# Optimization experiments

Measured on AMD Instinct MI355X. Metric: run time of the kernel, lower is better.

The kernel has to match this reference:

```python
import jax, jax.numpy as jnp
import numpy as np

B, L, S, H, E = 2, 2048, 2048, 16, 64


def setup_inputs() -> dict:
    key = jax.random.key(0)
    kq, kk, kv = jax.random.split(key, 3)
    queries = jax.random.normal(kq, (B, L, H, E), dtype=jnp.float32)
    keys = jax.random.normal(kk, (B, S, H, E), dtype=jnp.float32)
    values = jax.random.normal(kv, (B, S, H, E), dtype=jnp.float32)
    attn_mask = jnp.ones((B, 1, L, S), dtype=jnp.float32)  # >0.5 means attend
    return {"queries": queries, "keys": keys, "values": values, "attn_mask": attn_mask}


def reference(queries, keys, values, attn_mask):
    # queries: [B,L,H,E], keys/values: [B,S,H,E], attn_mask broadcastable to [B,H,L,S]
    E_ = queries.shape[-1]
    scale = 1.0 / np.sqrt(E_).astype(np.float32)
    scores = jnp.einsum('blhe,bshe->bhls', queries, keys)  # [B,H,L,S]
    large_negative = jnp.float32(-1e9)
    scores = scores + jnp.where(attn_mask > 0.5, jnp.float32(0.0), large_negative)
    A = jax.nn.softmax(scale * scores, axis=-1)  # dropout p=0.0 -> identity
    V = jnp.einsum('bhls,bshd->bhld', A, values)  # [B,H,L,D]
    return V
```

## Files before the change

### kernel.cpp

```cpp
#include <hip/hip_runtime.h>

typedef float    f32x4 __attribute__((ext_vector_type(4)));
typedef _Float16 f16x2 __attribute__((ext_vector_type(2)));
typedef _Float16 f16x4 __attribute__((ext_vector_type(4)));
typedef _Float16 f16x8 __attribute__((ext_vector_type(8)));
typedef int      i32x4 __attribute__((ext_vector_type(4)));

namespace {
constexpr int B_ = 2, L_ = 2048, S_ = 2048, H_ = 16, E_ = 64;
constexpr int MBLK = 128;
constexpr int NT = 64;
constexpr int NTILES = S_ / NT;

#define SCALE2f 0.1803368801111204f
#define MBIAS2f -1.8033688e8f

constexpr size_t KHOFF = (size_t)1 << 20;
constexpr size_t VHOFF = KHOFF + (size_t)B_ * H_ * S_ * E_ * 2;

__device__ __forceinline__ f16x2 cvt2(float a, float b) {
  return __builtin_bit_cast(f16x2, __builtin_amdgcn_cvt_pkrtz(a, b));
}
__device__ __forceinline__ int pkh(float a, float b) {
  return __builtin_bit_cast(int, __builtin_amdgcn_cvt_pkrtz(a, b));
}
union H8 { f16x8 v; i32x4 i; };
union H4 { f16x4 v; f16x2 h[2]; };

#define GLOAD_LDS16(g, l)                                              \
  __builtin_amdgcn_global_load_lds(                                    \
      (const __attribute__((address_space(1))) void*)(g),              \
      (__attribute__((address_space(3))) void*)(l), 16, 0, 0)
}

extern "C" __global__ __launch_bounds__(256)
void maskpack_kernel(const float* __restrict__ Mg, unsigned long long* __restrict__ Wb) {
  const int u = blockIdx.x * 256 + threadIdx.x;
  const float* src = Mg + (size_t)u * 16;
  unsigned m = 0;
#pragma unroll
  for (int i = 0; i < 4; ++i) {
    f32x4 x = *(const f32x4*)(src + i * 4);
#pragma unroll
    for (int c = 0; c < 4; ++c) m |= (x[c] > 0.5f ? 1u : 0u) << (i * 4 + c);
  }
  ((unsigned short*)Wb)[u] = (unsigned short)m;
}

extern "C" __global__ __launch_bounds__(256)
void kcvt_kernel(const float* __restrict__ Kg, _Float16* __restrict__ Kh) {
  const int idx = blockIdx.x * 256 + threadIdx.x;
  const int j = idx & 7;
  const int h = (idx >> 3) & (H_ - 1);
  const int s = (idx >> 7) & (S_ - 1);
  const int b = idx >> 18;
  const float* src = Kg + ((((size_t)b * S_ + s) * H_ + h) << 6) + j * 8;
  f32x4 x = *(const f32x4*)src, y = *(const f32x4*)(src + 4);
  i32x4 w = {pkh(x[0], x[1]), pkh(x[2], x[3]), pkh(y[0], y[1]), pkh(y[2], y[3])};
  *(i32x4*)(Kh + ((((size_t)b * H_ + h) * S_ + s) << 6) + j * 8) = w;
}

extern "C" __global__ __launch_bounds__(256)
void vcvt_kernel(const float* __restrict__ Vg, _Float16* __restrict__ Vh) {
  __shared__ _Float16 T[64][72];
  const int bid = blockIdx.x;
  const int st = bid & 31;
  const int h  = (bid >> 5) & (H_ - 1);
  const int b  = bid >> 9;
  const int t  = threadIdx.x;
  const int sl = t >> 2;
  const int e0 = (t & 3) << 4;
  const float* src = Vg + ((((size_t)b * S_ + st * 64 + sl) * H_ + h) << 6) + e0;
#pragma unroll
  for (int i = 0; i < 4; ++i) {
    f32x4 x = *(const f32x4*)(src + i * 4);
#pragma unroll
    for (int c = 0; c < 4; ++c) T[e0 + i * 4 + c][sl] = (_Float16)x[c];
  }
  __syncthreads();
  const int er = t >> 2;
  const int s0 = (t & 3) << 4;
  _Float16* dst = Vh + (((((size_t)b * H_ + h) << 6) + er) * S_) + st * 64 + s0;
  *(i32x4*)dst       = *(const i32x4*)&T[er][s0];
  *(i32x4*)(dst + 8) = *(const i32x4*)&T[er][s0 + 8];
}

extern "C" __global__ __launch_bounds__(512, 4)
void fattn_kernel(const float* __restrict__ Qg, const _Float16* __restrict__ Kh,
                  const _Float16* __restrict__ Vh, const unsigned long long* __restrict__ Wb,
                  float* __restrict__ Og) {
  __shared__ __align__(16) _Float16 Ks[2][NT][64];
  __shared__ __align__(16) _Float16 Vt[2][E_][64];

  const int tid  = threadIdx.x;
  const int wv   = tid >> 6;
  const int lane = tid & 63;
  const int qd   = lane >> 4;
  const int cl   = lane & 15;
  const int sw   = cl & 7;

  const int bid = blockIdx.x;
  const int qb  = bid >> 5;
  const int bh  = bid & 31;
  const int h   = bh & (H_ - 1);
  const int b   = bh >> 4;

  const int l0 = qb * MBLK + wv * 16;

  f16x8 qf[2];
  {
    const float* qp = Qg + ((((size_t)b * L_ + (l0 + cl)) * H_ + h) << 6);
#pragma unroll
    for (int kb = 0; kb < 2; ++kb) {
      const int e0 = qd * 8 + kb * 32;
      f32x4 x = *(const f32x4*)(qp + e0);
      f32x4 y = *(const f32x4*)(qp + e0 + 4);
      H8 u;
      u.i = (i32x4){pkh(x[0], x[1]), pkh(x[2], x[3]), pkh(y[0], y[1]), pkh(y[2], y[3])};
      qf[kb] = u.v;
    }
  }

  const int rl  = lane >> 3;
  const int gsl = lane & 7;
  const int gsw = gsl ^ rl;
  const _Float16* khb = Kh + ((((size_t)b * H_ + h) * S_) << 6);
  const _Float16* vhb = Vh + ((((size_t)b * H_ + h) << 6) * (size_t)S_);

  const unsigned long long* wbp = Wb + (((size_t)b * L_ + (l0 + cl)) << 5);

  auto dma = [&](int buf, int t) {
    const int r0 = wv * 8;
    const _Float16* ksrc = khb + (((size_t)(t * 64 + r0 + rl)) << 6) + gsw * 8;
    GLOAD_LDS16(ksrc, &Ks[buf][r0][0]);
    const _Float16* vsrc = vhb + (size_t)(r0 + rl) * S_ + t * 64 + gsw * 8;
    GLOAD_LDS16(vsrc, &Vt[buf][r0][0]);
  };

  const f32x4 zero4 = {0.f, 0.f, 0.f, 0.f};
  f32x4 acc[4];
#pragma unroll
  for (int et = 0; et < 4; ++et) acc[et] = zero4;
  f32x4 rs4 = zero4;

  dma(0, 0);
  unsigned long long mwcur = wbp[0];

  for (int t = 0; t < NTILES; ++t) {
    const int cb = t & 1;
    __syncthreads();

    if (t + 1 < NTILES) dma(cb ^ 1, t + 1);
    unsigned long long mwnext = 0;
    if (t + 1 < NTILES) mwnext = wbp[t + 1];

    f32x4 sc[4];
#pragma unroll
    for (int nt = 0; nt < 4; ++nt) {
      const _Float16* krow = &Ks[cb][nt * 16 + cl][0];
      const f16x8 a0 = *(const f16x8*)(krow + ((qd ^ sw) << 3));
      const f16x8 a1 = *(const f16x8*)(krow + (((qd + 4) ^ sw) << 3));
      f32x4 c = zero4;
      c = __builtin_amdgcn_mfma_f32_16x16x32_f16(a0, qf[0], c, 0, 0, 0);
      c = __builtin_amdgcn_mfma_f32_16x16x32_f16(a1, qf[1], c, 0, 0, 0);
      sc[nt] = c;
    }

    f16x4 pa[4];
    if (mwcur == ~0ull) {
#pragma unroll
      for (int nt = 0; nt < 4; ++nt) {
        f32x4 p;
#pragma unroll
        for (int r = 0; r < 4; ++r)
          p[r] = __builtin_amdgcn_exp2f(sc[nt][r] * SCALE2f);
        rs4 += p;
        H4 u;
        u.h[0] = cvt2(p[0], p[1]);
        u.h[1] = cvt2(p[2], p[3]);
        pa[nt] = u.v;
      }
    } else {
      const unsigned lo = (unsigned)mwcur;
      const unsigned hi = (unsigned)(mwcur >> 32);
#pragma unroll
      for (int nt = 0; nt < 4; ++nt) {
        const unsigned shm = ((nt < 2) ? lo : hi) >> ((nt & 1) * 16 + qd * 4);
        f32x4 p;
#pragma unroll
        for (int r = 0; r < 4; ++r) {
          const float bias = (shm & (1u << r)) ? 0.f : MBIAS2f;
          p[r] = __builtin_amdgcn_exp2f(__builtin_fmaf(sc[nt][r], SCALE2f, bias));
        }
        rs4 += p;
        H4 u;
        u.h[0] = cvt2(p[0], p[1]);
        u.h[1] = cvt2(p[2], p[3]);
        pa[nt] = u.v;
      }
    }

#pragma unroll
    for (int nt = 0; nt < 4; ++nt)
#pragma unroll
      for (int et = 0; et < 4; ++et) {
        const _Float16* vrow = &Vt[cb][et * 16 + cl][0];
        const f16x4 bv = *(const f16x4*)(vrow + ((((2 * nt + (qd >> 1)) ^ sw) << 3) + ((qd & 1) << 2)));
        acc[et] = __builtin_amdgcn_mfma_f32_16x16x16f16(pa[nt], bv, acc[et], 0, 0, 0);
      }

    mwcur = mwnext;
  }

  {
    float v = rs4[0] + rs4[1] + rs4[2] + rs4[3];
    v += __shfl_xor(v, 16, 64);
    v += __shfl_xor(v, 32, 64);
#pragma unroll
    for (int r = 0; r < 4; ++r) {
      const float invq = 1.0f / __shfl(v, qd * 4 + r, 64);
      const int l = l0 + qd * 4 + r;
      float* op = Og + ((((size_t)b * H_ + h) * L_ + l) << 6) + cl;
#pragma unroll
      for (int et = 0; et < 4; ++et) op[et * 16] = acc[et][r] * invq;
    }
  }
}

extern "C" void kernel_launch(void* const* d_in, const int* in_sizes, int n_in,
                              void* d_out, int out_size, void* d_ws, size_t ws_size,
                              hipStream_t stream) {
  const float* Q = (const float*)d_in[0];
  const float* K = (const float*)d_in[1];
  const float* V = (const float*)d_in[2];
  const float* M = (const float*)d_in[3];
  float* O = (float*)d_out;
  unsigned long long* Wb = (unsigned long long*)d_ws;
  _Float16* Khp = (_Float16*)((char*)d_ws + KHOFF);
  _Float16* Vhp = (_Float16*)((char*)d_ws + VHOFF);

  hipLaunchKernelGGL(maskpack_kernel, dim3(B_ * L_ * S_ / (16 * 256)), dim3(256), 0, stream, M, Wb);
  hipLaunchKernelGGL(kcvt_kernel, dim3(B_ * S_ * H_ * 8 / 256), dim3(256), 0, stream, K, Khp);
  hipLaunchKernelGGL(vcvt_kernel, dim3(B_ * H_ * (S_ / 64)), dim3(256), 0, stream, V, Vhp);
  hipLaunchKernelGGL(fattn_kernel, dim3(B_ * H_ * (L_ / MBLK)), dim3(512), 0, stream,
                     Q, Khp, Vhp, Wb, O);
}
```

Before: 166.6 us.

## Fuse prep kernels and triple-buffer K/V tiles with explicit waitcnt pipelining

The three preprocessing kernels (mask pack, K convert, V transpose-convert) become one launch that picks its branch by block index, cutting launch overhead. The attention loop moves from double to triple buffering of the K/V LDS tiles with a prefetch distance of two. It replaces __syncthreads with explicit s_waitcnt vmcnt(3) plus s_barrier and adds s_setprio around the MFMA phases. The extra buffer raises LDS use per block, which may limit occupancy, and the hand-written waitcnt depends on exactly how many loads the compiler emits.

```diff
diff --git a/kernel.cpp b/kernel.cpp
--- a/kernel.cpp
+++ b/kernel.cpp
@@ -34,63 +34,63 @@
 }
 
 extern "C" __global__ __launch_bounds__(256)
-void maskpack_kernel(const float* __restrict__ Mg, unsigned long long* __restrict__ Wb) {
-  const int u = blockIdx.x * 256 + threadIdx.x;
-  const float* src = Mg + (size_t)u * 16;
-  unsigned m = 0;
-#pragma unroll
-  for (int i = 0; i < 4; ++i) {
-    f32x4 x = *(const f32x4*)(src + i * 4);
-#pragma unroll
-    for (int c = 0; c < 4; ++c) m |= (x[c] > 0.5f ? 1u : 0u) << (i * 4 + c);
-  }
-  ((unsigned short*)Wb)[u] = (unsigned short)m;
-}
-
-extern "C" __global__ __launch_bounds__(256)
-void kcvt_kernel(const float* __restrict__ Kg, _Float16* __restrict__ Kh) {
-  const int idx = blockIdx.x * 256 + threadIdx.x;
-  const int j = idx & 7;
-  const int h = (idx >> 3) & (H_ - 1);
-  const int s = (idx >> 7) & (S_ - 1);
-  const int b = idx >> 18;
-  const float* src = Kg + ((((size_t)b * S_ + s) * H_ + h) << 6) + j * 8;
-  f32x4 x = *(const f32x4*)src, y = *(const f32x4*)(src + 4);
-  i32x4 w = {pkh(x[0], x[1]), pkh(x[2], x[3]), pkh(y[0], y[1]), pkh(y[2], y[3])};
-  *(i32x4*)(Kh + ((((size_t)b * H_ + h) * S_ + s) << 6) + j * 8) = w;
-}
-
-extern "C" __global__ __launch_bounds__(256)
-void vcvt_kernel(const float* __restrict__ Vg, _Float16* __restrict__ Vh) {
+void prep_kernel(const float* __restrict__ Kg, const float* __restrict__ Vg,
+                 const float* __restrict__ Mg, _Float16* __restrict__ Kh,
+                 _Float16* __restrict__ Vh, unsigned long long* __restrict__ Wb) {
   __shared__ _Float16 T[64][72];
   const int bid = blockIdx.x;
-  const int st = bid & 31;
-  const int h  = (bid >> 5) & (H_ - 1);
-  const int b  = bid >> 9;
-  const int t  = threadIdx.x;
-  const int sl = t >> 2;
-  const int e0 = (t & 3) << 4;
-  const float* src = Vg + ((((size_t)b * S_ + st * 64 + sl) * H_ + h) << 6) + e0;
-#pragma unroll
-  for (int i = 0; i < 4; ++i) {
-    f32x4 x = *(const f32x4*)(src + i * 4);
-#pragma unroll
-    for (int c = 0; c < 4; ++c) T[e0 + i * 4 + c][sl] = (_Float16)x[c];
-  }
-  __syncthreads();
-  const int er = t >> 2;
-  const int s0 = (t & 3) << 4;
-  _Float16* dst = Vh + (((((size_t)b * H_ + h) << 6) + er) * S_) + st * 64 + s0;
-  *(i32x4*)dst       = *(const i32x4*)&T[er][s0];
-  *(i32x4*)(dst + 8) = *(const i32x4*)&T[er][s0 + 8];
+  const int t   = threadIdx.x;
+
+  if (bid < 2048) {
+    const int idx = bid * 256 + t;
+    const int j = idx & 7;
+    const int h = (idx >> 3) & (H_ - 1);
+    const int s = (idx >> 7) & (S_ - 1);
+    const int b = idx >> 18;
+    const float* src = Kg + ((((size_t)b * S_ + s) * H_ + h) << 6) + j * 8;
+    f32x4 x = *(const f32x4*)src, y = *(const f32x4*)(src + 4);
+    i32x4 w = {pkh(x[0], x[1]), pkh(x[2], x[3]), pkh(y[0], y[1]), pkh(y[2], y[3])};
+    *(i32x4*)(Kh + ((((size_t)b * H_ + h) * S_ + s) << 6) + j * 8) = w;
+  } else if (bid < 4096) {
+    const int u = (bid - 2048) * 256 + t;
+    const float* src = Mg + (size_t)u * 16;
+    unsigned m = 0;
+#pragma unroll
+    for (int i = 0; i < 4; ++i) {
+      f32x4 x = *(const f32x4*)(src + i * 4);
+#pragma unroll
+      for (int c = 0; c < 4; ++c) m |= (x[c] > 0.5f ? 1u : 0u) << (i * 4 + c);
+    }
+    ((unsigned short*)Wb)[u] = (unsigned short)m;
+  } else {
+    const int vb = bid - 4096;
+    const int st = vb & 31;
+    const int h  = (vb >> 5) & (H_ - 1);
+    const int b  = vb >> 9;
+    const int sl = t >> 2;
+    const int e0 = (t & 3) << 4;
+    const float* src = Vg + ((((size_t)b * S_ + st * 64 + sl) * H_ + h) << 6) + e0;
+#pragma unroll
+    for (int i = 0; i < 4; ++i) {
+      f32x4 x = *(const f32x4*)(src + i * 4);
+#pragma unroll
+      for (int c = 0; c < 4; ++c) T[e0 + i * 4 + c][sl] = (_Float16)x[c];
+    }
+    __syncthreads();
+    const int er = t >> 2;
+    const int s0 = (t & 3) << 4;
+    _Float16* dst = Vh + (((((size_t)b * H_ + h) << 6) + er) * S_) + st * 64 + s0;
+    *(i32x4*)dst       = *(const i32x4*)&T[er][s0];
+    *(i32x4*)(dst + 8) = *(const i32x4*)&T[er][s0 + 8];
+  }
 }
 
 extern "C" __global__ __launch_bounds__(512, 4)
 void fattn_kernel(const float* __restrict__ Qg, const _Float16* __restrict__ Kh,
                   const _Float16* __restrict__ Vh, const unsigned long long* __restrict__ Wb,
                   float* __restrict__ Og) {
-  __shared__ __align__(16) _Float16 Ks[2][NT][64];
-  __shared__ __align__(16) _Float16 Vt[2][E_][64];
+  __shared__ __align__(16) _Float16 Ks[3][NT][64];
+  __shared__ __align__(16) _Float16 Vt[3][E_][64];
 
   const int tid  = threadIdx.x;
   const int wv   = tid >> 6;
@@ -143,21 +143,35 @@
   for (int et = 0; et < 4; ++et) acc[et] = zero4;
   f32x4 rs4 = zero4;
 
+  unsigned long long mwcur = wbp[0];
   dma(0, 0);
-  unsigned long long mwcur = wbp[0];
-
+  asm volatile("" ::: "memory");
+  __builtin_amdgcn_sched_barrier(0);
+  unsigned long long mwnext = wbp[1];
+  dma(1, 1);
+
+  int bc = 0;
   for (int t = 0; t < NTILES; ++t) {
-    const int cb = t & 1;
-    __syncthreads();
-
-    if (t + 1 < NTILES) dma(cb ^ 1, t + 1);
-    unsigned long long mwnext = 0;
-    if (t + 1 < NTILES) mwnext = wbp[t + 1];
+    __builtin_amdgcn_sched_barrier(0);
+    if (t < NTILES - 1)
+      asm volatile("s_waitcnt vmcnt(3) lgkmcnt(0)" ::: "memory");
+    else
+      asm volatile("s_waitcnt vmcnt(0) lgkmcnt(0)" ::: "memory");
+    __builtin_amdgcn_s_barrier();
+    __builtin_amdgcn_sched_barrier(0);
+
+    unsigned long long mwnext2 = 0;
+    if (t + 2 < NTILES) {
+      int b2 = bc + 2; if (b2 >= 3) b2 -= 3;
+      mwnext2 = wbp[t + 2];
+      dma(b2, t + 2);
+    }
 
     f32x4 sc[4];
+    __builtin_amdgcn_s_setprio(1);
 #pragma unroll
     for (int nt = 0; nt < 4; ++nt) {
-      const _Float16* krow = &Ks[cb][nt * 16 + cl][0];
+      const _Float16* krow = &Ks[bc][nt * 16 + cl][0];
       const f16x8 a0 = *(const f16x8*)(krow + ((qd ^ sw) << 3));
       const f16x8 a1 = *(const f16x8*)(krow + (((qd + 4) ^ sw) << 3));
       f32x4 c = zero4;
@@ -165,6 +179,7 @@
       c = __builtin_amdgcn_mfma_f32_16x16x32_f16(a1, qf[1], c, 0, 0, 0);
       sc[nt] = c;
     }
+    __builtin_amdgcn_s_setprio(0);
 
     f16x4 pa[4];
     if (mwcur == ~0ull) {
@@ -200,16 +215,20 @@
       }
     }
 
+    __builtin_amdgcn_s_setprio(1);
 #pragma unroll
     for (int nt = 0; nt < 4; ++nt)
 #pragma unroll
       for (int et = 0; et < 4; ++et) {
-        const _Float16* vrow = &Vt[cb][et * 16 + cl][0];
+        const _Float16* vrow = &Vt[bc][et * 16 + cl][0];
         const f16x4 bv = *(const f16x4*)(vrow + ((((2 * nt + (qd >> 1)) ^ sw) << 3) + ((qd & 1) << 2)));
         acc[et] = __builtin_amdgcn_mfma_f32_16x16x16f16(pa[nt], bv, acc[et], 0, 0, 0);
       }
+    __builtin_amdgcn_s_setprio(0);
 
     mwcur = mwnext;
+    mwnext = mwnext2;
+    bc = (bc + 1 == 3) ? 0 : bc + 1;
   }
 
   {
@@ -239,9 +258,7 @@
   _Float16* Khp = (_Float16*)((char*)d_ws + KHOFF);
   _Float16* Vhp = (_Float16*)((char*)d_ws + VHOFF);
 
-  hipLaunchKernelGGL(maskpack_kernel, dim3(B_ * L_ * S_ / (16 * 256)), dim3(256), 0, stream, M, Wb);
-  hipLaunchKernelGGL(kcvt_kernel, dim3(B_ * S_ * H_ * 8 / 256), dim3(256), 0, stream, K, Khp);
-  hipLaunchKernelGGL(vcvt_kernel, dim3(B_ * H_ * (S_ / 64)), dim3(256), 0, stream, V, Vhp);
+  hipLaunchKernelGGL(prep_kernel, dim3(5120), dim3(256), 0, stream, K, V, M, Khp, Vhp, Wb);
   hipLaunchKernelGGL(fattn_kernel, dim3(B_ * H_ * (L_ / MBLK)), dim3(512), 0, stream,
                      Q, Khp, Vhp, Wb, O);
 }
```

Result: no change. 168.3 us (+1.0%).
